# Kernel optimization log

Hardware: AMD Instinct MI355X
Metric: run time of the kernel (lower is better)

## Reference

```python
import jax, jax.numpy as jnp
import numpy as np

T, B = 64, 32
V, E, H = 32000, 1024, 1024


def setup_inputs() -> dict:
    key = jax.random.key(0)
    ks = jax.random.split(key, 8)
    return {
        "target_tokens": jax.random.randint(ks[0], (T, B), 0, V),
        "ground_truth": jax.random.randint(ks[1], (T, B), 0, V),
        "embedding": jax.random.normal(ks[2], (V, E), jnp.float32) * 0.02,
        "W_ih": jax.random.normal(ks[3], (E, 4 * H), jnp.float32) / np.sqrt(E),
        "W_hh": jax.random.normal(ks[4], (H, 4 * H), jnp.float32) / np.sqrt(H),
        "b": jnp.zeros((4 * H,), jnp.float32),
        "W_out": jax.random.normal(ks[5], (H, V), jnp.float32) / np.sqrt(H),
        "b_out": jnp.zeros((V,), jnp.float32),
    }


def _lstm_logits(emb, W_ih, W_hh, b, W_out, b_out):
    # emb: [T, B, E] time-major; initial state (H_C=None) -> zeros
    Bsz = emb.shape[1]
    h0 = jnp.zeros((Bsz, W_hh.shape[0]), emb.dtype)
    c0 = jnp.zeros_like(h0)
    # precompute input projection for all timesteps in one GEMM
    x_proj = jnp.einsum('tbe,eg->tbg', emb, W_ih) + b  # [T, B, 4H]

    def step(carry, xg):
        h, c = carry
        gates = xg + h @ W_hh  # [B, 4H]
        i, f, g, o = jnp.split(gates, 4, axis=-1)
        c = jax.nn.sigmoid(f) * c + jax.nn.sigmoid(i) * jnp.tanh(g)
        h = jax.nn.sigmoid(o) * jnp.tanh(c)
        return (h, c), h

    (_, _), hs = jax.lax.scan(step, (h0, c0), x_proj)  # hs: [T, B, H]
    logits = jnp.einsum('tbh,hv->tbv', hs, W_out) + b_out  # [T, B, V]
    return logits


def reference(target_tokens, ground_truth, embedding, W_ih, W_hh, b, W_out, b_out):
    emb = embedding[target_tokens]  # [T, B, E]
    logits = _lstm_logits(emb, W_ih, W_hh, b, W_out, b_out)
    logits2d = logits.reshape(-1, logits.shape[-1])  # [T*B, V]
    gt = ground_truth.reshape(-1)  # [T*B]
    logp = jax.nn.log_softmax(logits2d, axis=-1)
    nll = -jnp.take_along_axis(logp, gt[:, None], axis=1)[:, 0]
    return jnp.mean(nll)
```

## Files before the change

kernel.cpp:

```cpp
#include <hip/hip_runtime.h>
#include <hip/hip_bf16.h>

typedef unsigned short u16;
typedef unsigned long long ull;
typedef __attribute__((ext_vector_type(8))) short bf16x8;
typedef __attribute__((ext_vector_type(4))) float f32x4;
typedef __attribute__((ext_vector_type(4))) int i32x4;

#define NSLICE 500

__device__ __forceinline__ u16 f2bf(float x){
  unsigned b = __float_as_uint(x);
  return (u16)((b + 0x7FFFu + ((b>>16)&1u)) >> 16);
}
__device__ __forceinline__ float sigm(float x){ return 1.f/(1.f+__expf(-x)); }

__device__ __forceinline__ void gload_lds16(const void* g, void* l){
  __builtin_amdgcn_global_load_lds(
      (const __attribute__((address_space(1))) unsigned int*)g,
      (__attribute__((address_space(3))) unsigned int*)l, 16, 0, 0);
}
#define SWZ(row, kb) ((kb) ^ (((row)&7)<<4))

template<int OFF>
__device__ __forceinline__ i32x4 gload16_coh(const char* p){
  i32x4 d;
  asm volatile("global_load_dwordx4 %0, %1, off offset:%2 sc0 sc1"
               : "=v"(d) : "v"(p), "n"(OFF) : "memory");
  return d;
}

__device__ __forceinline__ void transpose_tile(
    const float* __restrict__ in, u16* __restrict__ out, int N, int K,
    int nb, int kb, float (*tile)[65])
{
  const int t = threadIdx.x;
#pragma unroll
  for (int i=0;i<4;++i){
    int idx = i*256 + t;
    int k = idx>>4, n4 = idx&15;
    const float4 v = *(const float4*)&in[(size_t)(kb+k)*N + nb + n4*4];
    tile[k][n4*4+0]=v.x; tile[k][n4*4+1]=v.y; tile[k][n4*4+2]=v.z; tile[k][n4*4+3]=v.w;
  }
  __syncthreads();
#pragma unroll
  for (int i=0;i<2;++i){
    int idx = i*256 + t;
    int n = idx>>3, k8 = idx&7;
    u16 tmp[8];
#pragma unroll
    for (int jj=0;jj<8;++jj) tmp[jj] = f2bf(tile[k8*8+jj][n]);
    *(ulonglong2*)&out[(size_t)(nb+n)*K + kb + k8*8] = *(ulonglong2*)tmp;
  }
}

__global__ __launch_bounds__(256) void prep_kernel(
    const float* __restrict__ Wout, const float* __restrict__ Wih,
    const float* __restrict__ Whh, const int* __restrict__ tok,
    const float* __restrict__ emb,
    u16* __restrict__ WoutT, u16* __restrict__ WihT, u16* __restrict__ WhhT,
    u16* __restrict__ embg, float* __restrict__ zbuf, float* __restrict__ out0)
{
  __shared__ float tile[64][65];
  const int b = blockIdx.x;
  if (b < 8000){
    transpose_tile(Wout, WoutT, 32000, 1024, (b%500)*64, (b/500)*64, tile);
  } else if (b < 9024){
    const int i = b - 8000;
    transpose_tile(Wih, WihT, 4096, 1024, (i&63)*64, (i>>6)*64, tile);
  } else if (b < 10048){
    const int i = b - 9024;
    transpose_tile(Whh, WhhT, 4096, 1024, (i&63)*64, (i>>6)*64, tile);
  } else if (b < 12096){
    const int r = b - 10048, t = threadIdx.x;
    const int trow = tok[r];
    const float4 v = *(const float4*)(emb + (size_t)trow*1024 + t*4);
    ull o = (ull)f2bf(v.x) | ((ull)f2bf(v.y)<<16) | ((ull)f2bf(v.z)<<32) | ((ull)f2bf(v.w)<<48);
    *(ull*)(embg + (size_t)r*1024 + t*4) = o;
  } else {
    const int i = (b - 12096)*256 + threadIdx.x;
    if (i < 65792) zbuf[i] = 0.f;
    if (i == 0) out0[0] = 0.f;
  }
}

__device__ __forceinline__ void gemm_tile_128(
    const u16* __restrict__ A, const u16* __restrict__ BT,
    int rowbase, int colbase, u16* As, u16* Bs, f32x4 (&acc)[4][4])
{
  const int tid = threadIdx.x;
  const int lane = tid & 63;
  const int wm = (tid>>6)>>1, wn = (tid>>6)&1;
#pragma unroll
  for (int m=0;m<4;++m)
#pragma unroll
    for (int n=0;n<4;++n) acc[m][n] = (f32x4){0.f,0.f,0.f,0.f};

  for (int kb = 0; kb < 1024; kb += 64){
    __syncthreads();
#pragma unroll
    for (int i=0;i<4;++i){
      const int row = i*32 + (tid>>3);
      const int kf  = (tid&7)*16;
      gload_lds16((const char*)(A  + (size_t)(rowbase+row)*1024 + kb) + SWZ(row,kf),
                  (char*)As + (i*256+tid)*16);
      gload_lds16((const char*)(BT + (size_t)(colbase+row)*1024 + kb) + SWZ(row,kf),
                  (char*)Bs + (i*256+tid)*16);
    }
    __syncthreads();
#pragma unroll
    for (int ks=0;ks<2;++ks){
      bf16x8 af[4], bfr[4];
      const int kbyte = ks*64 + (lane>>4)*16;
#pragma unroll
      for (int m=0;m<4;++m){
        const int row = wm*64 + m*16 + (lane&15);
        af[m] = *(const bf16x8*)((const char*)As + row*128 + SWZ(row,kbyte));
      }
#pragma unroll
      for (int n=0;n<4;++n){
        const int col = wn*64 + n*16 + (lane&15);
        bfr[n] = *(const bf16x8*)((const char*)Bs + col*128 + SWZ(col,kbyte));
      }
#pragma unroll
      for (int m=0;m<4;++m)
#pragma unroll
        for (int n=0;n<4;++n)
          acc[m][n] = __builtin_amdgcn_mfma_f32_16x16x32_bf16(af[m], bfr[n], acc[m][n], 0,0,0);
    }
  }
}

__global__ __launch_bounds__(256,2) void xproj_gemm(
    const u16* __restrict__ Aemb, const u16* __restrict__ WihT,
    const float* __restrict__ bias, float* __restrict__ xgP)
{
  __shared__ u16 As[8192], Bs[8192];
  const int fb = blockIdx.x;
  const int g = (fb&7)*64 + (fb>>3);
  const int ct = g>>4, rt = g&15;
  const int rowbase = rt*128, colbase = ct*128;
  const int tid = threadIdx.x, lane = tid&63;
  const int wm = (tid>>6)>>1, wn = (tid>>6)&1;
  f32x4 acc[4][4];
  gemm_tile_128(Aemb, WihT, rowbase, colbase, As, Bs, acc);
  float bv[4];
#pragma unroll
  for (int n=0;n<4;++n) bv[n] = bias[colbase + wn*64 + n*16 + (lane&15)];
#pragma unroll
  for (int m=0;m<4;++m)
#pragma unroll
    for (int n=0;n<4;++n)
#pragma unroll
      for (int r=0;r<4;++r){
        const int row = rowbase + wm*64 + m*16 + (lane>>4)*4 + r;
        const int col = colbase + wn*64 + n*16 + (lane&15);
        const int tt = row>>5, b = row&31;
        const int q = col>>10, hcol = col&1023;
        xgP[(size_t)(((tt*256 + (hcol>>2))*32 + b)*16 + (hcol&3)*4 + q)] = acc[m][n][r] + bv[n];
      }
}

__global__ __launch_bounds__(256,1) void lstm_persistent(
    const u16* __restrict__ WhhT, const float* __restrict__ xgP,
    u16* __restrict__ hb0, u16* __restrict__ hb1, u16* __restrict__ hsbf,
    unsigned* __restrict__ bar)
{
  __shared__ float red[4*32*16];
  const int cb = blockIdx.x;
  const int tid = threadIdx.x, lane = tid&63, w = tid>>6;
  const int f = lane & 15;
  const int kfrag = (lane>>4)*8;
  const int gcol = cb*4 + (f&3) + 1024*(f>>2);
  const int bb = tid>>2, j = tid&3;
  const int w8 = w*8;

  bf16x8 wreg[8];
#pragma unroll
  for (int i=0;i<8;++i)
    wreg[i] = *(const bf16x8*)(WhhT + (size_t)gcol*1024 + (w8+i)*32 + kfrag);

  float creg = 0.f;
  float4 x4 = {0.f,0.f,0.f,0.f};
  if (tid < 128)
    x4 = *(const float4*)(xgP + ((size_t)0*256 + cb)*512 + bb*16 + j*4);

  for (int t=0; t<64; ++t){
    const u16* hin = (t&1) ? hb1 : hb0;
    u16*      hout = (t&1) ? hb0 : hb1;

    const char* p0 = (const char*)(hin + (size_t)f*1024 + w8*32 + kfrag);
    const char* p1 = p0 + 32768;
    i32x4 h0[8], h1[8];
    h0[0]=gload16_coh<  0>(p0); h0[1]=gload16_coh< 64>(p0);
    h0[2]=gload16_coh<128>(p0); h0[3]=gload16_coh<192>(p0);
    h0[4]=gload16_coh<256>(p0); h0[5]=gload16_coh<320>(p0);
    h0[6]=gload16_coh<384>(p0); h0[7]=gload16_coh<448>(p0);
    h1[0]=gload16_coh<  0>(p1); h1[1]=gload16_coh< 64>(p1);
    h1[2]=gload16_coh<128>(p1); h1[3]=gload16_coh<192>(p1);
    h1[4]=gload16_coh<256>(p1); h1[5]=gload16_coh<320>(p1);
    h1[6]=gload16_coh<384>(p1); h1[7]=gload16_coh<448>(p1);
    asm volatile("s_waitcnt vmcnt(0)" ::: "memory");
    __builtin_amdgcn_sched_barrier(0);

    f32x4 acc0 = (f32x4){0.f,0.f,0.f,0.f};
    f32x4 acc1 = (f32x4){0.f,0.f,0.f,0.f};
#pragma unroll
    for (int i=0;i<8;++i){
      acc0 = __builtin_amdgcn_mfma_f32_16x16x32_bf16(
                 __builtin_bit_cast(bf16x8, h0[i]), wreg[i], acc0, 0,0,0);
      acc1 = __builtin_amdgcn_mfma_f32_16x16x32_bf16(
                 __builtin_bit_cast(bf16x8, h1[i]), wreg[i], acc1, 0,0,0);
    }
#pragma unroll
    for (int r=0;r<4;++r){
      red[w*512 + ((lane>>4)*4 + r)*16 + f]      = acc0[r];
      red[w*512 + (16 + (lane>>4)*4 + r)*16 + f] = acc1[r];
    }
    __syncthreads();
    unsigned hu = 0;
    if (tid < 128){
      float g4[4];
#pragma unroll
      for (int q=0;q<4;++q){
        const int ff = j + 4*q;
        g4[q] = red[0*512 + bb*16 + ff] + red[1*512 + bb*16 + ff]
              + red[2*512 + bb*16 + ff] + red[3*512 + bb*16 + ff];
      }
      g4[0] += x4.x; g4[1] += x4.y; g4[2] += x4.z; g4[3] += x4.w;
      const float iv = sigm(g4[0]), fv = sigm(g4[1]);
      const float gv = tanhf(g4[2]), ov = sigm(g4[3]);
      const float cn = fv*creg + iv*gv;
      const float hv = ov*tanhf(cn);
      creg = cn;
      hu = (unsigned)f2bf(hv);
    }
    const unsigned v1 = __shfl_down(hu, 1, 64);
    const unsigned v2 = __shfl_down(hu, 2, 64);
    const unsigned v3 = __shfl_down(hu, 3, 64);
    const ull p = (ull)hu | ((ull)v1<<16) | ((ull)v2<<32) | ((ull)v3<<48);
    if (tid < 128 && j == 0){
      __hip_atomic_store((ull*)&hout[bb*1024 + cb*4], p,
                         __ATOMIC_RELAXED, __HIP_MEMORY_SCOPE_AGENT);
    }
    if (t < 63){
      __syncthreads();
      if (tid == 0)
        __hip_atomic_fetch_add(&bar[(cb & 7)*32], 1u,
                               __ATOMIC_RELAXED, __HIP_MEMORY_SCOPE_AGENT);
      if (tid < 128 && j == 0)
        *(ull*)&hsbf[(size_t)t*32768 + bb*1024 + cb*4] = p;
      if (tid < 128)
        x4 = *(const float4*)(xgP + ((size_t)(t+1)*256 + cb)*512 + bb*16 + j*4);
      if (tid == 0){
        const unsigned target = (unsigned)(t+1)*32u;
        for (;;){
          bool ok = true;
#pragma unroll
          for (int i=0;i<8;++i)
            ok &= (__hip_atomic_load(&bar[i*32], __ATOMIC_RELAXED,
                                     __HIP_MEMORY_SCOPE_AGENT) >= target);
          if (ok) break;
          __builtin_amdgcn_s_sleep(2);
        }
        asm volatile("" ::: "memory");
      }
      __syncthreads();
    } else {
      if (tid < 128 && j == 0)
        *(ull*)&hsbf[(size_t)63*32768 + bb*1024 + cb*4] = p;
    }
  }
}

__global__ __launch_bounds__(256) void lstm_step_mfma(
    const u16* __restrict__ hin, const u16* __restrict__ WhhT,
    const float* __restrict__ xgPt, float* __restrict__ ccell,
    u16* __restrict__ hout, u16* __restrict__ hs_t)
{
  __shared__ float red[4*32*16];
  const int cb = blockIdx.x;
  const int tid = threadIdx.x, lane = tid&63, w = tid>>6;
  const int f = lane & 15;
  const int gcol = cb*4 + (f&3) + 1024*(f>>2);
  const int kfrag = (lane>>4)*8;
  f32x4 acc0 = (f32x4){0.f,0.f,0.f,0.f};
  f32x4 acc1 = (f32x4){0.f,0.f,0.f,0.f};
  const int kb0 = w*256;
#pragma unroll
  for (int kk=0; kk<256; kk+=32){
    const int k = kb0 + kk + kfrag;
    const bf16x8 bfr = *(const bf16x8*)(WhhT + (size_t)gcol*1024 + k);
    const bf16x8 a0  = *(const bf16x8*)(hin + (size_t)f*1024 + k);
    const bf16x8 a1  = *(const bf16x8*)(hin + (size_t)(16+f)*1024 + k);
    acc0 = __builtin_amdgcn_mfma_f32_16x16x32_bf16(a0, bfr, acc0, 0,0,0);
    acc1 = __builtin_amdgcn_mfma_f32_16x16x32_bf16(a1, bfr, acc1, 0,0,0);
  }
#pragma unroll
  for (int r=0;r<4;++r){
    red[w*512 + ((lane>>4)*4 + r)*16 + f]      = acc0[r];
    red[w*512 + (16 + (lane>>4)*4 + r)*16 + f] = acc1[r];
  }
  __syncthreads();
  if (tid < 128){
    const int bb = tid >> 2, j = tid & 3;
    const int hcol = cb*4 + j;
    const float4 x4 = *(const float4*)(xgPt + (size_t)cb*512 + bb*16 + j*4);
    float g4[4];
#pragma unroll
    for (int q=0;q<4;++q){
      const int ff = j + 4*q;
      g4[q] = red[0*512 + bb*16 + ff] + red[1*512 + bb*16 + ff]
            + red[2*512 + bb*16 + ff] + red[3*512 + bb*16 + ff];
    }
    g4[0] += x4.x; g4[1] += x4.y; g4[2] += x4.z; g4[3] += x4.w;
    const float iv = sigm(g4[0]), fv = sigm(g4[1]);
    const float gv = tanhf(g4[2]), ov = sigm(g4[3]);
    const int hidx = bb*1024 + hcol;
    const float cn = fv*ccell[hidx] + iv*gv;
    const float hv = ov*tanhf(cn);
    ccell[hidx] = cn;
    const u16 hb = f2bf(hv);
    hout[hidx] = hb;
    hs_t[hidx] = hb;
  }
}

__global__ __launch_bounds__(256,2) void logits_gemm_lse(
    const u16* __restrict__ hs, const u16* __restrict__ WoutT,
    const float* __restrict__ bout, const int* __restrict__ gt,
    float* __restrict__ partm, float* __restrict__ parts, float* __restrict__ gtl)
{
  __shared__ u16 As[8192], Bs[8192];
  __shared__ int gts[128];
  const int fb = blockIdx.x;
  const int g = (fb&7)*500 + (fb>>3);
  const int vt = g>>4, rt = g&15;
  const int rowbase = rt*128, colbase = vt*128;
  const int tid = threadIdx.x, lane = tid&63;
  const int wm = (tid>>6)>>1, wn = (tid>>6)&1;
  if (tid < 128) gts[tid] = gt[rowbase + tid];
  f32x4 acc[4][4];
  gemm_tile_128(hs, WoutT, rowbase, colbase, As, Bs, acc);
  float bv[4];
#pragma unroll
  for (int n=0;n<4;++n) bv[n] = bout[colbase + wn*64 + n*16 + (lane&15)];
#pragma unroll
  for (int m=0;m<4;++m)
#pragma unroll
    for (int n=0;n<4;++n)
#pragma unroll
      for (int r=0;r<4;++r) acc[m][n][r] += bv[n];
  float rm[4][4], rs[4][4];
#pragma unroll
  for (int m=0;m<4;++m)
#pragma unroll
    for (int r=0;r<4;++r){
      float mx = fmaxf(fmaxf(acc[m][0][r],acc[m][1][r]), fmaxf(acc[m][2][r],acc[m][3][r]));
      mx = fmaxf(mx, __shfl_xor(mx,1,16));
      mx = fmaxf(mx, __shfl_xor(mx,2,16));
      mx = fmaxf(mx, __shfl_xor(mx,4,16));
      mx = fmaxf(mx, __shfl_xor(mx,8,16));
      float sv = __expf(acc[m][0][r]-mx) + __expf(acc[m][1][r]-mx)
               + __expf(acc[m][2][r]-mx) + __expf(acc[m][3][r]-mx);
      sv += __shfl_xor(sv,1,16);
      sv += __shfl_xor(sv,2,16);
      sv += __shfl_xor(sv,4,16);
      sv += __shfl_xor(sv,8,16);
      rm[m][r]=mx; rs[m][r]=sv;
    }
  const int slice = vt*2 + wn;
  if ((lane&15)==0){
#pragma unroll
    for (int m=0;m<4;++m)
#pragma unroll
      for (int r=0;r<4;++r){
        const int rloc = wm*64 + m*16 + (lane>>4)*4 + r;
        partm[(size_t)slice*2048 + rowbase + rloc] = rm[m][r];
        parts[(size_t)slice*2048 + rowbase + rloc] = rs[m][r];
      }
  }
#pragma unroll
  for (int m=0;m<4;++m)
#pragma unroll
    for (int r=0;r<4;++r){
      const int rloc = wm*64 + m*16 + (lane>>4)*4 + r;
      const int gg = gts[rloc] - colbase - wn*64;
      if (gg >= 0 && gg < 64 && (gg&15)==(lane&15)){
        const int n = gg>>4;
        const float val = (n==0)?acc[m][0][r] : (n==1)?acc[m][1][r]
                        : (n==2)?acc[m][2][r] : acc[m][3][r];
        gtl[rowbase+rloc] = val;
      }
    }
}

__global__ __launch_bounds__(256) void lse_finalize2(
    const float* __restrict__ partm, const float* __restrict__ parts,
    const float* __restrict__ gtl, float* __restrict__ out)
{
  __shared__ float red[4];
  const int r = blockIdx.x*256 + threadIdx.x;
  float m = -1e30f;
  for (int i=0;i<NSLICE;++i) m = fmaxf(m, partm[(size_t)i*2048 + r]);
  float s = 0.f;
  for (int i=0;i<NSLICE;++i) s += parts[(size_t)i*2048 + r]*__expf(partm[(size_t)i*2048 + r]-m);
  float v = (m + logf(s) - gtl[r]) * (1.0f/2048.0f);
#pragma unroll
  for (int off=32;off>=1;off>>=1) v += __shfl_down(v, off, 64);
  if ((threadIdx.x&63)==0) red[threadIdx.x>>6]=v;
  __syncthreads();
  if (threadIdx.x==0) atomicAdd(out, red[0]+red[1]+red[2]+red[3]);
}

extern "C" void kernel_launch(void* const* d_in, const int* in_sizes, int n_in,
                              void* d_out, int out_size, void* d_ws, size_t ws_size,
                              hipStream_t stream)
{
  const int*   tok  = (const int*)d_in[0];
  const int*   gt   = (const int*)d_in[1];
  const float* emb  = (const float*)d_in[2];
  const float* Wih  = (const float*)d_in[3];
  const float* Whh  = (const float*)d_in[4];
  const float* bias = (const float*)d_in[5];
  const float* Wout = (const float*)d_in[6];
  const float* bout = (const float*)d_in[7];
  float* out = (float*)d_out;

  char* base = (char*)d_ws;
  u16*   WoutT = (u16*)base;            base += 65536000;
  u16*   WihT  = (u16*)base;            base += 8388608;
  u16*   WhhT  = (u16*)base;            base += 8388608;
  u16*   embg  = (u16*)base;            base += 4194304;
  float* xgP   = (float*)base;          base += 33554432;
  u16*   hsbf  = (u16*)base;            base += 4194304;
  float* cbuf  = (float*)base;          base += 131072;
  u16*   hb0   = (u16*)base;            base += 65536;
  u16*   hb1   = (u16*)base;            base += 65536;
  unsigned* bar = (unsigned*)base;      base += 1024;
  float* partm = (float*)base;          base += 4096000;
  float* parts = (float*)base;          base += 4096000;
  float* gtl   = (float*)base;          base += 8192;

  prep_kernel<<<12353, 256, 0, stream>>>(Wout, Wih, Whh, tok, emb,
                                         WoutT, WihT, WhhT, embg, cbuf, out);

  xproj_gemm<<<512, 256, 0, stream>>>(embg, WihT, bias, xgP);

  int coop = 0;
  hipDeviceGetAttribute(&coop, hipDeviceAttributeCooperativeLaunch, 0);
  if (coop){
    void* args[] = {(void*)&WhhT, (void*)&xgP, (void*)&hb0, (void*)&hb1,
                    (void*)&hsbf, (void*)&bar};
    hipLaunchCooperativeKernel((const void*)lstm_persistent,
                               dim3(256), dim3(256), args, 0, stream);
  } else {
    for (int t = 0; t < 64; ++t){
      const u16* hin = (t & 1) ? hb1 : hb0;
      u16*      hout = (t & 1) ? hb0 : hb1;
      lstm_step_mfma<<<256, 256, 0, stream>>>(hin, WhhT,
          xgP + (size_t)t*131072, cbuf, hout, hsbf + (size_t)t*32768);
    }
  }

  logits_gemm_lse<<<4000, 256, 0, stream>>>(hsbf, WoutT, bout, gt, partm, parts, gtl);
  lse_finalize2<<<8, 256, 0, stream>>>(partm, parts, gtl, out);
}
```

Before: 642.7 us.

## Run output-projection GEMM in FP8 with FP8 W_out and hidden states

Converts the transposed W_out to FP8 during prep and has the LSTM also emit its hidden states as FP8. The logits GEMM then uses the 16x16x128 FP8 MFMA with byte-sized LDS tiles. The aim is to halve the memory traffic for W_out and hs and to raise matrix throughput in the dominant GEMM. The cost is lower numerical precision in the logits, which feed the log-softmax loss.

```diff
diff --git a/kernel.cpp b/kernel.cpp
--- a/kernel.cpp
+++ b/kernel.cpp
@@ -2,10 +2,12 @@
 #include <hip/hip_bf16.h>
 
 typedef unsigned short u16;
+typedef unsigned char u8;
 typedef unsigned long long ull;
 typedef __attribute__((ext_vector_type(8))) short bf16x8;
 typedef __attribute__((ext_vector_type(4))) float f32x4;
 typedef __attribute__((ext_vector_type(4))) int i32x4;
+typedef __attribute__((ext_vector_type(8))) int i32x8;
 
 #define NSLICE 500
 
@@ -30,9 +32,13 @@
   return d;
 }
 
-__device__ __forceinline__ void transpose_tile(
-    const float* __restrict__ in, u16* __restrict__ out, int N, int K,
-    int nb, int kb, float (*tile)[65])
+__device__ __forceinline__ f32x4 mfma_f8(i32x8 a, i32x8 b, f32x4 c){
+  asm("v_mfma_f32_16x16x128_f8f6f4 %0, %1, %2, %0" : "+v"(c) : "v"(a), "v"(b));
+  return c;
+}
+
+__device__ __forceinline__ void load_tile64(
+    const float* __restrict__ in, int N, int nb, int kb, float (*tile)[65])
 {
   const int t = threadIdx.x;
 #pragma unroll
@@ -43,42 +49,56 @@
     tile[k][n4*4+0]=v.x; tile[k][n4*4+1]=v.y; tile[k][n4*4+2]=v.z; tile[k][n4*4+3]=v.w;
   }
   __syncthreads();
-#pragma unroll
-  for (int i=0;i<2;++i){
-    int idx = i*256 + t;
-    int n = idx>>3, k8 = idx&7;
-    u16 tmp[8];
-#pragma unroll
-    for (int jj=0;jj<8;++jj) tmp[jj] = f2bf(tile[k8*8+jj][n]);
-    *(ulonglong2*)&out[(size_t)(nb+n)*K + kb + k8*8] = *(ulonglong2*)tmp;
-  }
 }
 
 __global__ __launch_bounds__(256) void prep_kernel(
     const float* __restrict__ Wout, const float* __restrict__ Wih,
     const float* __restrict__ Whh, const int* __restrict__ tok,
     const float* __restrict__ emb,
-    u16* __restrict__ WoutT, u16* __restrict__ WihT, u16* __restrict__ WhhT,
+    u8* __restrict__ WoutT8, u16* __restrict__ WihT, u16* __restrict__ WhhT,
     u16* __restrict__ embg, float* __restrict__ zbuf, float* __restrict__ out0)
 {
   __shared__ float tile[64][65];
   const int b = blockIdx.x;
+  const int t = threadIdx.x;
   if (b < 8000){
-    transpose_tile(Wout, WoutT, 32000, 1024, (b%500)*64, (b/500)*64, tile);
-  } else if (b < 9024){
-    const int i = b - 8000;
-    transpose_tile(Wih, WihT, 4096, 1024, (i&63)*64, (i>>6)*64, tile);
+    const int nb = (b%500)*64, kb = (b/500)*64;
+    load_tile64(Wout, 32000, nb, kb, tile);
+#pragma unroll
+    for (int i=0;i<2;++i){
+      int idx = i*256 + t;
+      int n = idx>>3, k8 = idx&7;
+      float v0=tile[k8*8+0][n], v1=tile[k8*8+1][n], v2=tile[k8*8+2][n], v3=tile[k8*8+3][n];
+      float v4=tile[k8*8+4][n], v5=tile[k8*8+5][n], v6=tile[k8*8+6][n], v7=tile[k8*8+7][n];
+      unsigned w0 = __builtin_amdgcn_cvt_pk_fp8_f32(v0, v1, 0, 0);
+      w0 = __builtin_amdgcn_cvt_pk_fp8_f32(v2, v3, w0, 1);
+      unsigned w1 = __builtin_amdgcn_cvt_pk_fp8_f32(v4, v5, 0, 0);
+      w1 = __builtin_amdgcn_cvt_pk_fp8_f32(v6, v7, w1, 1);
+      *(ull*)&WoutT8[(size_t)(nb+n)*1024 + kb + k8*8] = (ull)w0 | ((ull)w1<<32);
+    }
   } else if (b < 10048){
-    const int i = b - 9024;
-    transpose_tile(Whh, WhhT, 4096, 1024, (i&63)*64, (i>>6)*64, tile);
+    const int i = (b < 9024) ? b - 8000 : b - 9024;
+    const float* in = (b < 9024) ? Wih : Whh;
+    u16* out = (b < 9024) ? WihT : WhhT;
+    const int nb = (i&63)*64, kb = (i>>6)*64;
+    load_tile64(in, 4096, nb, kb, tile);
+#pragma unroll
+    for (int ii=0;ii<2;++ii){
+      int idx = ii*256 + t;
+      int n = idx>>3, k8 = idx&7;
+      u16 tmp[8];
+#pragma unroll
+      for (int jj=0;jj<8;++jj) tmp[jj] = f2bf(tile[k8*8+jj][n]);
+      *(ulonglong2*)&out[(size_t)(nb+n)*1024 + kb + k8*8] = *(ulonglong2*)tmp;
+    }
   } else if (b < 12096){
-    const int r = b - 10048, t = threadIdx.x;
+    const int r = b - 10048;
     const int trow = tok[r];
     const float4 v = *(const float4*)(emb + (size_t)trow*1024 + t*4);
     ull o = (ull)f2bf(v.x) | ((ull)f2bf(v.y)<<16) | ((ull)f2bf(v.z)<<32) | ((ull)f2bf(v.w)<<48);
     *(ull*)(embg + (size_t)r*1024 + t*4) = o;
   } else {
-    const int i = (b - 12096)*256 + threadIdx.x;
+    const int i = (b - 12096)*256 + t;
     if (i < 65792) zbuf[i] = 0.f;
     if (i == 0) out0[0] = 0.f;
   }
@@ -163,7 +183,7 @@
 
 __global__ __launch_bounds__(256,1) void lstm_persistent(
     const u16* __restrict__ WhhT, const float* __restrict__ xgP,
-    u16* __restrict__ hb0, u16* __restrict__ hb1, u16* __restrict__ hsbf,
+    u16* __restrict__ hb0, u16* __restrict__ hb1, u8* __restrict__ hsf8,
     unsigned* __restrict__ bar)
 {
   __shared__ float red[4*32*16];
@@ -218,7 +238,7 @@
       red[w*512 + (16 + (lane>>4)*4 + r)*16 + f] = acc1[r];
     }
     __syncthreads();
-    unsigned hu = 0;
+    unsigned hu = 0, fb8 = 0;
     if (tid < 128){
       float g4[4];
 #pragma unroll
@@ -234,11 +254,16 @@
       const float hv = ov*tanhf(cn);
       creg = cn;
       hu = (unsigned)f2bf(hv);
+      fb8 = __builtin_amdgcn_cvt_pk_fp8_f32(hv, 0.f, 0, 0) & 0xffu;
     }
     const unsigned v1 = __shfl_down(hu, 1, 64);
     const unsigned v2 = __shfl_down(hu, 2, 64);
     const unsigned v3 = __shfl_down(hu, 3, 64);
     const ull p = (ull)hu | ((ull)v1<<16) | ((ull)v2<<32) | ((ull)v3<<48);
+    const unsigned f1 = __shfl_down(fb8, 1, 64);
+    const unsigned f2 = __shfl_down(fb8, 2, 64);
+    const unsigned f3 = __shfl_down(fb8, 3, 64);
+    const unsigned pf = fb8 | (f1<<8) | (f2<<16) | (f3<<24);
     if (tid < 128 && j == 0){
       __hip_atomic_store((ull*)&hout[bb*1024 + cb*4], p,
                          __ATOMIC_RELAXED, __HIP_MEMORY_SCOPE_AGENT);
@@ -249,7 +274,7 @@
         __hip_atomic_fetch_add(&bar[(cb & 7)*32], 1u,
                                __ATOMIC_RELAXED, __HIP_MEMORY_SCOPE_AGENT);
       if (tid < 128 && j == 0)
-        *(ull*)&hsbf[(size_t)t*32768 + bb*1024 + cb*4] = p;
+        *(unsigned*)&hsf8[(size_t)t*32768 + bb*1024 + cb*4] = pf;
       if (tid < 128)
         x4 = *(const float4*)(xgP + ((size_t)(t+1)*256 + cb)*512 + bb*16 + j*4);
       if (tid == 0){
@@ -268,7 +293,7 @@
       __syncthreads();
     } else {
       if (tid < 128 && j == 0)
-        *(ull*)&hsbf[(size_t)63*32768 + bb*1024 + cb*4] = p;
+        *(unsigned*)&hsf8[(size_t)63*32768 + bb*1024 + cb*4] = pf;
     }
   }
 }
@@ -276,7 +301,7 @@
 __global__ __launch_bounds__(256) void lstm_step_mfma(
     const u16* __restrict__ hin, const u16* __restrict__ WhhT,
     const float* __restrict__ xgPt, float* __restrict__ ccell,
-    u16* __restrict__ hout, u16* __restrict__ hs_t)
+    u16* __restrict__ hout, u8* __restrict__ hs8_t)
 {
   __shared__ float red[4*32*16];
   const int cb = blockIdx.x;
@@ -320,18 +345,17 @@
     const float cn = fv*ccell[hidx] + iv*gv;
     const float hv = ov*tanhf(cn);
     ccell[hidx] = cn;
-    const u16 hb = f2bf(hv);
-    hout[hidx] = hb;
-    hs_t[hidx] = hb;
+    hout[hidx] = f2bf(hv);
+    hs8_t[hidx] = (u8)(__builtin_amdgcn_cvt_pk_fp8_f32(hv, 0.f, 0, 0) & 0xffu);
   }
 }
 
 __global__ __launch_bounds__(256,2) void logits_gemm_lse(
-    const u16* __restrict__ hs, const u16* __restrict__ WoutT,
+    const u8* __restrict__ hs8, const u8* __restrict__ WoutT8,
     const float* __restrict__ bout, const int* __restrict__ gt,
     float* __restrict__ partm, float* __restrict__ parts, float* __restrict__ gtl)
 {
-  __shared__ u16 As[8192], Bs[8192];
+  __shared__ u8 As8[16384], Bs8[16384];
   __shared__ int gts[128];
   const int fb = blockIdx.x;
   const int g = (fb&7)*500 + (fb>>3);
@@ -341,7 +365,48 @@
   const int wm = (tid>>6)>>1, wn = (tid>>6)&1;
   if (tid < 128) gts[tid] = gt[rowbase + tid];
   f32x4 acc[4][4];
-  gemm_tile_128(hs, WoutT, rowbase, colbase, As, Bs, acc);
+#pragma unroll
+  for (int m=0;m<4;++m)
+#pragma unroll
+    for (int n=0;n<4;++n) acc[m][n] = (f32x4){0.f,0.f,0.f,0.f};
+
+  for (int kb = 0; kb < 8; ++kb){
+    __syncthreads();
+#pragma unroll
+    for (int i=0;i<4;++i){
+      const int row = i*32 + (tid>>3);
+      const int kf  = (tid&7)*16;
+      gload_lds16((const char*)(hs8    + (size_t)(rowbase+row)*1024 + kb*128) + SWZ(row,kf),
+                  (char*)As8 + (i*256+tid)*16);
+      gload_lds16((const char*)(WoutT8 + (size_t)(colbase+row)*1024 + kb*128) + SWZ(row,kf),
+                  (char*)Bs8 + (i*256+tid)*16);
+    }
+    __syncthreads();
+    const int kbyte = (lane>>4)*32;
+    i32x8 af[4], bfr[4];
+#pragma unroll
+    for (int m=0;m<4;++m){
+      const int row = wm*64 + m*16 + (lane&15);
+      union { i32x8 v8; i32x4 v4[2]; } u;
+      u.v4[0] = *(const i32x4*)(As8 + row*128 + SWZ(row, kbyte));
+      u.v4[1] = *(const i32x4*)(As8 + row*128 + SWZ(row, kbyte+16));
+      af[m] = u.v8;
+    }
+#pragma unroll
+    for (int n=0;n<4;++n){
+      const int col = wn*64 + n*16 + (lane&15);
+      union { i32x8 v8; i32x4 v4[2]; } u;
+      u.v4[0] = *(const i32x4*)(Bs8 + col*128 + SWZ(col, kbyte));
+      u.v4[1] = *(const i32x4*)(Bs8 + col*128 + SWZ(col, kbyte+16));
+      bfr[n] = u.v8;
+    }
+#pragma unroll
+    for (int m=0;m<4;++m)
+#pragma unroll
+      for (int n=0;n<4;++n)
+        acc[m][n] = mfma_f8(af[m], bfr[n], acc[m][n]);
+  }
+
   float bv[4];
 #pragma unroll
   for (int n=0;n<4;++n) bv[n] = bout[colbase + wn*64 + n*16 + (lane&15)];
@@ -428,12 +493,12 @@
   float* out = (float*)d_out;
 
   char* base = (char*)d_ws;
-  u16*   WoutT = (u16*)base;            base += 65536000;
+  u8*    WoutT8 = (u8*)base;            base += 32768000;
   u16*   WihT  = (u16*)base;            base += 8388608;
   u16*   WhhT  = (u16*)base;            base += 8388608;
   u16*   embg  = (u16*)base;            base += 4194304;
   float* xgP   = (float*)base;          base += 33554432;
-  u16*   hsbf  = (u16*)base;            base += 4194304;
+  u8*    hsf8  = (u8*)base;             base += 2097152;
   float* cbuf  = (float*)base;          base += 131072;
   u16*   hb0   = (u16*)base;            base += 65536;
   u16*   hb1   = (u16*)base;            base += 65536;
@@ -443,7 +508,7 @@
   float* gtl   = (float*)base;          base += 8192;
 
   prep_kernel<<<12353, 256, 0, stream>>>(Wout, Wih, Whh, tok, emb,
-                                         WoutT, WihT, WhhT, embg, cbuf, out);
+                                         WoutT8, WihT, WhhT, embg, cbuf, out);
 
   xproj_gemm<<<512, 256, 0, stream>>>(embg, WihT, bias, xgP);
 
@@ -451,7 +516,7 @@
   hipDeviceGetAttribute(&coop, hipDeviceAttributeCooperativeLaunch, 0);
   if (coop){
     void* args[] = {(void*)&WhhT, (void*)&xgP, (void*)&hb0, (void*)&hb1,
-                    (void*)&hsbf, (void*)&bar};
+                    (void*)&hsf8, (void*)&bar};
     hipLaunchCooperativeKernel((const void*)lstm_persistent,
                                dim3(256), dim3(256), args, 0, stream);
   } else {
@@ -459,10 +524,10 @@
       const u16* hin = (t & 1) ? hb1 : hb0;
       u16*      hout = (t & 1) ? hb0 : hb1;
       lstm_step_mfma<<<256, 256, 0, stream>>>(hin, WhhT,
-          xgP + (size_t)t*131072, cbuf, hout, hsbf + (size_t)t*32768);
-    }
-  }
-
-  logits_gemm_lse<<<4000, 256, 0, stream>>>(hsbf, WoutT, bout, gt, partm, parts, gtl);
+          xgP + (size_t)t*131072, cbuf, hout, hsf8 + (size_t)t*32768);
+    }
+  }
+
+  logits_gemm_lse<<<4000, 256, 0, stream>>>(hsf8, WoutT8, bout, gt, partm, parts, gtl);
   lse_finalize2<<<8, 256, 0, stream>>>(partm, parts, gtl, out);
 }
```

Result: faster. 570.4 us (-11.3%).
